# Optimization experiments

Measured on AMD Instinct MI355X. Metric: run time of the kernel, lower is better.

Reference implementation:

```python
import jax, jax.numpy as jnp
import numpy as np

B, T, C, H = 2, 2048, 1024, 16
D = C // H  # 64 per-head dim


def setup_inputs() -> dict:
    key = jax.random.key(0)
    ks = jax.random.split(key, 9)
    s = 1.0 / np.sqrt(C)
    return {
        "query_src": jax.random.normal(ks[0], (B, T, C), jnp.float32),
        "key_src": jax.random.normal(ks[1], (B, T, C), jnp.float32),
        "value_src": jax.random.normal(ks[2], (B, T, C), jnp.float32),
        "Wq": jax.random.normal(ks[3], (C, C), jnp.float32) * s,
        "Wk": jax.random.normal(ks[4], (C, C), jnp.float32) * s,
        "Wv": jax.random.normal(ks[5], (C, C), jnp.float32) * s,
        "Wo": jax.random.normal(ks[6], (C, C), jnp.float32) * s,
        "bo": jax.random.normal(ks[7], (C,), jnp.float32) * s,
    }


def reference(query_src, key_src, value_src, Wq, Wk, Wv, Wo, bo):
    # Linear layers: y = x @ W.T (torch nn.Linear convention)
    q = jnp.einsum('btc,dc->btd', query_src, Wq).reshape(B, T, H, D).transpose(0, 2, 1, 3)
    k = jnp.einsum('btc,dc->btd', key_src, Wk).reshape(B, T, H, D).transpose(0, 2, 1, 3)
    v = jnp.einsum('btc,dc->btd', value_src, Wv).reshape(B, T, H, D).transpose(0, 2, 1, 3)
    # scores: [B, H, T, T]
    scores = jnp.einsum('bhqd,bhkd->bhqk', q, k)
    # FAITHFUL quirk: original divides by d**(-0.5) => multiplies by sqrt(D)
    scores = scores * jnp.sqrt(jnp.asarray(D, scores.dtype))
    # FAITHFUL quirk: softmax over dim=1 == the HEAD axis
    attn = jax.nn.softmax(scores, axis=1)
    # dropout is identity in eval mode
    out = jnp.einsum('bhqk,bhkd->bhqd', attn, v)  # [B,H,T,D]
    out = out.transpose(0, 2, 1, 3).reshape(B, T, C)
    return jnp.einsum('btc,dc->btd', out, Wo) + bo
```

## Files before the change

kernel.cpp:

```cpp
#include <hip/hip_runtime.h>
#include <cmath>

namespace {

constexpr int B_ = 2;
constexpr int T_ = 2048;
constexpr int C_ = 1024;
constexpr int H_ = 16;
constexpr int D_ = 64;

typedef _Float16 half8 __attribute__((ext_vector_type(8)));
typedef _Float16 half4 __attribute__((ext_vector_type(4)));
typedef float f32x4 __attribute__((ext_vector_type(4)));

__device__ inline f32x4 vmax4(f32x4 a, f32x4 b) {
  f32x4 r;
  r[0] = fmaxf(a[0], b[0]); r[1] = fmaxf(a[1], b[1]);
  r[2] = fmaxf(a[2], b[2]); r[3] = fmaxf(a[3], b[3]);
  return r;
}

__device__ __forceinline__ void gload16(const _Float16* g, _Float16* l) {
  __builtin_amdgcn_global_load_lds(
      (const __attribute__((address_space(1))) unsigned int*)g,
      (__attribute__((address_space(3))) unsigned int*)l, 16, 0, 0);
}

__device__ __forceinline__ void lds_barrier() {
  __builtin_amdgcn_sched_barrier(0);
  asm volatile("s_waitcnt lgkmcnt(0)" ::: "memory");
  __builtin_amdgcn_s_barrier();
  __builtin_amdgcn_sched_barrier(0);
}

__global__ __launch_bounds__(256)
void cast7(const float* __restrict__ xq, const float* __restrict__ xk,
           const float* __restrict__ xv, const float* __restrict__ wq,
           const float* __restrict__ wk, const float* __restrict__ wv,
           const float* __restrict__ wo,
           _Float16* __restrict__ dxq, _Float16* __restrict__ dxk,
           _Float16* __restrict__ dxv, _Float16* __restrict__ dwq,
           _Float16* __restrict__ dwk, _Float16* __restrict__ dwv,
           _Float16* __restrict__ dwo) {
  constexpr size_t NX = (size_t)4 << 20;
  constexpr size_t NW = (size_t)1 << 20;
  size_t g = ((size_t)blockIdx.x * 256 + threadIdx.x) * 8;
  const float* s; _Float16* d; size_t off;
  if      (g <     NX)          { s = xq; d = dxq; off = g; }
  else if (g < 2 * NX)          { s = xk; d = dxk; off = g - NX; }
  else if (g < 3 * NX)          { s = xv; d = dxv; off = g - 2 * NX; }
  else if (g < 3 * NX + NW)     { s = wq; d = dwq; off = g - 3 * NX; }
  else if (g < 3 * NX + 2 * NW) { s = wk; d = dwk; off = g - 3 * NX - NW; }
  else if (g < 3 * NX + 3 * NW) { s = wv; d = dwv; off = g - 3 * NX - 2 * NW; }
  else                          { s = wo; d = dwo; off = g - 3 * NX - 3 * NW; }
  const float4 a = *(const float4*)(s + off);
  const float4 b = *(const float4*)(s + off + 4);
  half8 h;
  h[0] = (_Float16)a.x; h[1] = (_Float16)a.y; h[2] = (_Float16)a.z; h[3] = (_Float16)a.w;
  h[4] = (_Float16)b.x; h[5] = (_Float16)b.y; h[6] = (_Float16)b.z; h[7] = (_Float16)b.w;
  *(half8*)(d + off) = h;
}

__global__ __launch_bounds__(256, 3)
void gemm_f16nt(const _Float16* __restrict__ A0, const _Float16* __restrict__ A1,
                const _Float16* __restrict__ A2,
                const _Float16* __restrict__ W0, const _Float16* __restrict__ W1,
                const _Float16* __restrict__ W2,
                _Float16* __restrict__ Y0, _Float16* __restrict__ Y1,
                _Float16* __restrict__ Y2,
                float* __restrict__ Yf, const float* __restrict__ bias,
                int K, int N, int mode, float qsc) {
  __shared__ _Float16 sA[128 * 32];
  __shared__ _Float16 sW[128 * 32];

  const int tid  = threadIdx.x;
  const int lane = tid & 63;
  const int w    = tid >> 6;
  const int l15  = lane & 15;
  const int quad = lane >> 4;
  const int z    = blockIdx.z;
  const _Float16* A = (z == 0) ? A0 : (z == 1) ? A1 : A2;
  const _Float16* W = (z == 0) ? W0 : (z == 1) ? W1 : W2;
  _Float16*       Y = (z == 0) ? Y0 : (z == 1) ? Y1 : Y2;

  const int m0 = blockIdx.y * 128;
  const int n0 = blockIdx.x * 128;

  const int Rb  = lane >> 2;
  const int pch = lane & 3;
  const int lch = pch ^ ((Rb >> 1) & 3);
  const int swr = (l15 >> 1) & 3;

  f32x4 acc[4][4];
#pragma unroll
  for (int mt = 0; mt < 4; ++mt)
#pragma unroll
    for (int nt = 0; nt < 4; ++nt)
      acc[mt][nt] = (f32x4){0.f, 0.f, 0.f, 0.f};

  const int wm = (w >> 1) * 64;
  const int wn = (w & 1) * 64;

  for (int k0 = 0; k0 < K; k0 += 32) {
    __syncthreads();
#pragma unroll
    for (int j = 0; j < 2; ++j) {
      const int seg = w * 32 + j * 16;
      gload16(A + (size_t)(m0 + seg + Rb) * K + k0 + lch * 8, &sA[seg * 32]);
      gload16(W + (size_t)(n0 + seg + Rb) * K + k0 + lch * 8, &sW[seg * 32]);
    }
    __syncthreads();

    half8 af[4], wf[4];
#pragma unroll
    for (int mt = 0; mt < 4; ++mt) {
      const int R = wm + mt * 16 + l15;
      af[mt] = *(const half8*)&sA[R * 32 + (quad ^ swr) * 8];
    }
#pragma unroll
    for (int nt = 0; nt < 4; ++nt) {
      const int R = wn + nt * 16 + l15;
      wf[nt] = *(const half8*)&sW[R * 32 + (quad ^ swr) * 8];
    }
#pragma unroll
    for (int mt = 0; mt < 4; ++mt)
#pragma unroll
      for (int nt = 0; nt < 4; ++nt)
        acc[mt][nt] = __builtin_amdgcn_mfma_f32_16x16x32_f16(wf[nt], af[mt], acc[mt][nt], 0, 0, 0);
  }

  const float ysc = (mode == 0 && z == 0) ? qsc : 1.f;
#pragma unroll
  for (int mt = 0; mt < 4; ++mt)
#pragma unroll
    for (int nt = 0; nt < 4; ++nt) {
      const int m = m0 + wm + mt * 16 + l15;
      const int n = n0 + wn + nt * 16 + quad * 4;
      if (mode == 2) {
        float4 v;
        v.x = acc[mt][nt][0] + bias[n + 0];
        v.y = acc[mt][nt][1] + bias[n + 1];
        v.z = acc[mt][nt][2] + bias[n + 2];
        v.w = acc[mt][nt][3] + bias[n + 3];
        *(float4*)(Yf + (size_t)m * N + n) = v;
      } else {
        half4 hv;
#pragma unroll
        for (int r = 0; r < 4; ++r) hv[r] = (_Float16)(acc[mt][nt][r] * ysc);
        *(half4*)(Y + (size_t)m * N + n) = hv;
      }
    }
}

__global__ __launch_bounds__(256)
void transpose_v(const _Float16* __restrict__ Vh, _Float16* __restrict__ Vt) {
  constexpr int PAD = 1028;
  __shared__ _Float16 tile[16][PAD];
  const int b  = blockIdx.x >> 7;
  const int kt = blockIdx.x & 127;
  const int tid = threadIdx.x;

#pragma unroll
  for (int j = 0; j < 8; ++j) {
    const int ch = tid + 256 * j;
    const int t  = ch >> 7;
    const int c8 = ch & 127;
    *(half8*)&tile[t][c8 * 8] =
        *(const half8*)(Vh + ((size_t)b * T_ + kt * 16 + t) * C_ + c8 * 8);
  }
  __syncthreads();

#pragma unroll
  for (int j = 0; j < 8; ++j) {
    const int cc = tid + 256 * j;
    const int h  = cc >> 7;
    const int d  = (cc >> 1) & 63;
    const int th = (cc & 1) * 8;
    const int c  = h * 64 + d;
    half4 va, vb4;
#pragma unroll
    for (int i = 0; i < 4; ++i) va[i]  = tile[th + i][c];
#pragma unroll
    for (int i = 0; i < 4; ++i) vb4[i] = tile[th + 4 + i][c];
    const size_t base = (((size_t)b * H_ + h) * 128 + kt) * 1024 +
                        (size_t)((d & 15) * 64 + (th >> 2) * 16 + (d >> 4) * 4);
    *(half4*)(Vt + base) = va;
    *(half4*)(Vt + base + 16) = vb4;
  }
}

__global__ __launch_bounds__(256, 2)
void attn_mfma(const _Float16* __restrict__ Qhp, const _Float16* __restrict__ Khp,
               const _Float16* __restrict__ Vtp, _Float16* __restrict__ OP,
               int nsplit) {
  __shared__ f32x4 red[2][2][4][64];

  const int tid  = threadIdx.x;
  const int lane = tid & 63;
  const int w    = tid >> 6;
  const int l15  = lane & 15;
  const int quad = lane >> 4;
  const int cell = quad * 16 + l15;

  const int nbq   = B_ * (T_ / 16);
  const int split = blockIdx.x / nbq;
  const int bq    = blockIdx.x % nbq;
  const int b  = bq >> 7;
  const int q0 = (bq & 127) << 4;

  const size_t qrow = ((size_t)b * T_ + q0 + l15) * C_;

  half8 qh[4][2];
#pragma unroll
  for (int hl = 0; hl < 4; ++hl)
#pragma unroll
    for (int kk = 0; kk < 2; ++kk)
      qh[hl][kk] = *(const half8*)(Qhp + qrow + (w * 4 + hl) * 64 + kk * 32 + quad * 8);

  f32x4 oacc[4][4];
#pragma unroll
  for (int hl = 0; hl < 4; ++hl)
#pragma unroll
    for (int mt = 0; mt < 4; ++mt)
      oacc[hl][mt] = (f32x4){0.f, 0.f, 0.f, 0.f};

  const int kpb  = T_ / nsplit;
  const int k_lo = split * kpb;
  const int jt   = kpb / 16;

  const _Float16* vbase = Vtp + ((size_t)b * H_ + w * 4) * (128 * 1024) +
                          (size_t)(l15 * 64 + quad * 16);

  half8 akA[4][2], akB[4][2];

  auto loadK = [&](half8 (&buf)[4][2], int k0) {
    const size_t krow = ((size_t)b * T_ + k0 + l15) * C_;
#pragma unroll
    for (int hl = 0; hl < 4; ++hl)
#pragma unroll
      for (int kk = 0; kk < 2; ++kk)
        buf[hl][kk] = *(const half8*)(Khp + krow + (w * 4 + hl) * 64 + kk * 32 + quad * 8);
  };

  auto tile = [&](int j, half8 (&cur)[4][2], half8 (&nxt)[4][2]) {
    const int k0 = k_lo + j * 16;
    const int kt = k0 >> 4;
    const int p  = j & 1;

    f32x4 s[4];
#pragma unroll
    for (int hl = 0; hl < 4; ++hl) s[hl] = (f32x4){0.f, 0.f, 0.f, 0.f};
    __builtin_amdgcn_s_setprio(1);
#pragma unroll
    for (int hl = 0; hl < 4; ++hl)
#pragma unroll
      for (int kk = 0; kk < 2; ++kk)
        s[hl] = __builtin_amdgcn_mfma_f32_16x16x32_f16(cur[hl][kk], qh[hl][kk], s[hl], 0, 0, 0);
    __builtin_amdgcn_s_setprio(0);

    half8 avh[4][2];
#pragma unroll
    for (int hl = 0; hl < 4; ++hl) {
      const _Float16* vb = vbase + (size_t)hl * (128 * 1024) + (size_t)kt * 1024;
      avh[hl][0] = *(const half8*)(vb);
      avh[hl][1] = *(const half8*)(vb + 8);
    }
    __builtin_amdgcn_sched_barrier(0);
    if (j + 1 < jt) loadK(nxt, k0 + 16);
    __builtin_amdgcn_sched_barrier(0);

    red[p][0][w][cell] = vmax4(vmax4(s[0], s[1]), vmax4(s[2], s[3]));
    lds_barrier();
    const f32x4 gmax = vmax4(vmax4(red[p][0][0][cell], red[p][0][1][cell]),
                             vmax4(red[p][0][2][cell], red[p][0][3][cell]));
    f32x4 ps = (f32x4){0.f, 0.f, 0.f, 0.f};
#pragma unroll
    for (int hl = 0; hl < 4; ++hl)
#pragma unroll
      for (int r = 0; r < 4; ++r) {
        const float ev = __expf(s[hl][r] - gmax[r]);
        s[hl][r] = ev;
        ps[r] += ev;
      }
    red[p][1][w][cell] = ps;
    lds_barrier();
    const f32x4 gs = red[p][1][0][cell] + red[p][1][1][cell] +
                     red[p][1][2][cell] + red[p][1][3][cell];
    f32x4 inv;
#pragma unroll
    for (int r = 0; r < 4; ++r) inv[r] = 1.f / gs[r];

    half4 pf[4];
#pragma unroll
    for (int hl = 0; hl < 4; ++hl)
#pragma unroll
      for (int r = 0; r < 4; ++r)
        pf[hl][r] = (_Float16)(s[hl][r] * inv[r]);

    __builtin_amdgcn_s_setprio(1);
#pragma unroll
    for (int hl = 0; hl < 4; ++hl) {
      const half4 v0 = __builtin_shufflevector(avh[hl][0], avh[hl][0], 0, 1, 2, 3);
      const half4 v1 = __builtin_shufflevector(avh[hl][0], avh[hl][0], 4, 5, 6, 7);
      const half4 v2 = __builtin_shufflevector(avh[hl][1], avh[hl][1], 0, 1, 2, 3);
      const half4 v3 = __builtin_shufflevector(avh[hl][1], avh[hl][1], 4, 5, 6, 7);
      oacc[hl][0] = __builtin_amdgcn_mfma_f32_16x16x16f16(v0, pf[hl], oacc[hl][0], 0, 0, 0);
      oacc[hl][1] = __builtin_amdgcn_mfma_f32_16x16x16f16(v1, pf[hl], oacc[hl][1], 0, 0, 0);
      oacc[hl][2] = __builtin_amdgcn_mfma_f32_16x16x16f16(v2, pf[hl], oacc[hl][2], 0, 0, 0);
      oacc[hl][3] = __builtin_amdgcn_mfma_f32_16x16x16f16(v3, pf[hl], oacc[hl][3], 0, 0, 0);
    }
    __builtin_amdgcn_s_setprio(0);
  };

  loadK(akA, k_lo);
  for (int j = 0; j < jt; j += 2) {
    tile(j,     akA, akB);
    tile(j + 1, akB, akA);
  }

  _Float16* op = OP + (size_t)split * ((size_t)B_ * T_ * C_);
  const size_t orow = ((size_t)b * T_ + q0 + l15) * C_;
#pragma unroll
  for (int hl = 0; hl < 4; ++hl)
#pragma unroll
    for (int mt = 0; mt < 4; ++mt) {
      half4 hv;
#pragma unroll
      for (int r = 0; r < 4; ++r) hv[r] = (_Float16)oacc[hl][mt][r];
      *(half4*)(op + orow + (w * 4 + hl) * 64 + mt * 16 + quad * 4) = hv;
    }
}

__global__ __launch_bounds__(256)
void reduce_oh(const _Float16* __restrict__ OP, _Float16* __restrict__ AOh,
               int nsplit, size_t n) {
  const size_t i = ((size_t)blockIdx.x * 256 + threadIdx.x) * 8;
  float a[8] = {};
  for (int s = 0; s < nsplit; ++s) {
    const half8 v = *(const half8*)(OP + (size_t)s * n + i);
#pragma unroll
    for (int r = 0; r < 8; ++r) a[r] += (float)v[r];
  }
  half8 o;
#pragma unroll
  for (int r = 0; r < 8; ++r) o[r] = (_Float16)a[r];
  *(half8*)(AOh + i) = o;
}

}

extern "C" void kernel_launch(void* const* d_in, const int* in_sizes, int n_in,
                              void* d_out, int out_size, void* d_ws, size_t ws_size,
                              hipStream_t stream) {
  const float* xq = (const float*)d_in[0];
  const float* xk = (const float*)d_in[1];
  const float* xv = (const float*)d_in[2];
  const float* Wq = (const float*)d_in[3];
  const float* Wk = (const float*)d_in[4];
  const float* Wv = (const float*)d_in[5];
  const float* Wo = (const float*)d_in[6];
  const float* bo = (const float*)d_in[7];
  float* out = (float*)d_out;

  const size_t MB   = 1ull << 20;
  const size_t nBTC = (size_t)B_ * T_ * C_;

  char* wsb = (char*)d_ws;
  _Float16* Qh  = (_Float16*)(wsb + 0 * MB);
  _Float16* Kh  = (_Float16*)(wsb + 8 * MB);
  _Float16* Vt  = (_Float16*)(wsb + 16 * MB);
  _Float16* vh  = (_Float16*)(wsb + 24 * MB);
  _Float16* AOh = (_Float16*)(wsb + 24 * MB);
  _Float16* xqh = (_Float16*)(wsb + 32 * MB);
  _Float16* xkh = (_Float16*)(wsb + 40 * MB);
  _Float16* xvh = (_Float16*)(wsb + 48 * MB);
  _Float16* OP  = (_Float16*)(wsb + 32 * MB);
  _Float16* Wqh = (_Float16*)(wsb + 64 * MB);
  _Float16* Wkh = (_Float16*)(wsb + 66 * MB);
  _Float16* Wvh = (_Float16*)(wsb + 68 * MB);
  _Float16* Woh = (_Float16*)(wsb + 70 * MB);

  const int nsplit = 4;
  const int M = B_ * T_;
  dim3 blk(256);

  cast7<<<dim3(8192), blk, 0, stream>>>(xq, xk, xv, Wq, Wk, Wv, Wo,
                                        xqh, xkh, xvh, Wqh, Wkh, Wvh, Woh);

  gemm_f16nt<<<dim3(C_ / 128, M / 128, 3), blk, 0, stream>>>(
      xqh, xkh, xvh, Wqh, Wkh, Wvh, Qh, Kh, vh,
      nullptr, nullptr, C_, C_, 0, 8.f);

  transpose_v<<<dim3(B_ * 128), blk, 0, stream>>>(vh, Vt);

  attn_mfma<<<dim3(B_ * (T_ / 16) * nsplit), blk, 0, stream>>>(Qh, Kh, Vt, OP, nsplit);

  reduce_oh<<<dim3((unsigned)(nBTC / 2048)), blk, 0, stream>>>(OP, AOh, nsplit, nBTC);

  gemm_f16nt<<<dim3(C_ / 128, M / 128, 1), blk, 0, stream>>>(
      AOh, nullptr, nullptr, Woh, nullptr, nullptr, nullptr, nullptr, nullptr,
      out, bo, C_, C_, 2, 1.f);
}
```

Measured before the change: 424.3 us.

## Remap attention blocks per XCD for L2 reuse and drop K double-buffering

```diff
diff --git a/kernel.cpp b/kernel.cpp
--- a/kernel.cpp
+++ b/kernel.cpp
@@ -24,13 +24,6 @@
   __builtin_amdgcn_global_load_lds(
       (const __attribute__((address_space(1))) unsigned int*)g,
       (__attribute__((address_space(3))) unsigned int*)l, 16, 0, 0);
-}
-
-__device__ __forceinline__ void lds_barrier() {
-  __builtin_amdgcn_sched_barrier(0);
-  asm volatile("s_waitcnt lgkmcnt(0)" ::: "memory");
-  __builtin_amdgcn_s_barrier();
-  __builtin_amdgcn_sched_barrier(0);
 }
 
 __global__ __launch_bounds__(256)
@@ -191,8 +184,7 @@
 
 __global__ __launch_bounds__(256, 2)
 void attn_mfma(const _Float16* __restrict__ Qhp, const _Float16* __restrict__ Khp,
-               const _Float16* __restrict__ Vtp, _Float16* __restrict__ OP,
-               int nsplit) {
+               const _Float16* __restrict__ Vtp, _Float16* __restrict__ OP) {
   __shared__ f32x4 red[2][2][4][64];
 
   const int tid  = threadIdx.x;
@@ -202,11 +194,11 @@
   const int quad = lane >> 4;
   const int cell = quad * 16 + l15;
 
-  const int nbq   = B_ * (T_ / 16);
-  const int split = blockIdx.x / nbq;
-  const int bq    = blockIdx.x % nbq;
-  const int b  = bq >> 7;
-  const int q0 = (bq & 127) << 4;
+  const int xcd   = blockIdx.x & 7;
+  const int qi    = blockIdx.x >> 3;
+  const int b     = xcd & 1;
+  const int split = xcd >> 1;
+  const int q0    = qi << 4;
 
   const size_t qrow = ((size_t)b * T_ + q0 + l15) * C_;
 
@@ -215,7 +207,8 @@
   for (int hl = 0; hl < 4; ++hl)
 #pragma unroll
     for (int kk = 0; kk < 2; ++kk)
-      qh[hl][kk] = *(const half8*)(Qhp + qrow + (w * 4 + hl) * 64 + kk * 32 + quad * 8);
+      qh[hl][kk] = __builtin_nontemporal_load(
+          (const half8*)(Qhp + qrow + (w * 4 + hl) * 64 + kk * 32 + quad * 8));
 
   f32x4 oacc[4][4];
 #pragma unroll
@@ -224,53 +217,46 @@
     for (int mt = 0; mt < 4; ++mt)
       oacc[hl][mt] = (f32x4){0.f, 0.f, 0.f, 0.f};
 
-  const int kpb  = T_ / nsplit;
+  const int kpb  = T_ / 4;
   const int k_lo = split * kpb;
   const int jt   = kpb / 16;
 
   const _Float16* vbase = Vtp + ((size_t)b * H_ + w * 4) * (128 * 1024) +
                           (size_t)(l15 * 64 + quad * 16);
 
-  half8 akA[4][2], akB[4][2];
-
-  auto loadK = [&](half8 (&buf)[4][2], int k0) {
-    const size_t krow = ((size_t)b * T_ + k0 + l15) * C_;
-#pragma unroll
-    for (int hl = 0; hl < 4; ++hl)
-#pragma unroll
-      for (int kk = 0; kk < 2; ++kk)
-        buf[hl][kk] = *(const half8*)(Khp + krow + (w * 4 + hl) * 64 + kk * 32 + quad * 8);
-  };
-
-  auto tile = [&](int j, half8 (&cur)[4][2], half8 (&nxt)[4][2]) {
+  for (int j = 0; j < jt; ++j) {
     const int k0 = k_lo + j * 16;
     const int kt = k0 >> 4;
     const int p  = j & 1;
-
-    f32x4 s[4];
-#pragma unroll
-    for (int hl = 0; hl < 4; ++hl) s[hl] = (f32x4){0.f, 0.f, 0.f, 0.f};
-    __builtin_amdgcn_s_setprio(1);
+    const size_t krow = ((size_t)b * T_ + k0 + l15) * C_;
+
+    half8 akh[4][2];
+    half8 avh[4][2];
 #pragma unroll
     for (int hl = 0; hl < 4; ++hl)
 #pragma unroll
       for (int kk = 0; kk < 2; ++kk)
-        s[hl] = __builtin_amdgcn_mfma_f32_16x16x32_f16(cur[hl][kk], qh[hl][kk], s[hl], 0, 0, 0);
-    __builtin_amdgcn_s_setprio(0);
-
-    half8 avh[4][2];
+        akh[hl][kk] = *(const half8*)(Khp + krow + (w * 4 + hl) * 64 + kk * 32 + quad * 8);
 #pragma unroll
     for (int hl = 0; hl < 4; ++hl) {
       const _Float16* vb = vbase + (size_t)hl * (128 * 1024) + (size_t)kt * 1024;
       avh[hl][0] = *(const half8*)(vb);
       avh[hl][1] = *(const half8*)(vb + 8);
     }
-    __builtin_amdgcn_sched_barrier(0);
-    if (j + 1 < jt) loadK(nxt, k0 + 16);
-    __builtin_amdgcn_sched_barrier(0);
+
+    f32x4 s[4];
+#pragma unroll
+    for (int hl = 0; hl < 4; ++hl) s[hl] = (f32x4){0.f, 0.f, 0.f, 0.f};
+    __builtin_amdgcn_s_setprio(1);
+#pragma unroll
+    for (int hl = 0; hl < 4; ++hl)
+#pragma unroll
+      for (int kk = 0; kk < 2; ++kk)
+        s[hl] = __builtin_amdgcn_mfma_f32_16x16x32_f16(akh[hl][kk], qh[hl][kk], s[hl], 0, 0, 0);
+    __builtin_amdgcn_s_setprio(0);
 
     red[p][0][w][cell] = vmax4(vmax4(s[0], s[1]), vmax4(s[2], s[3]));
-    lds_barrier();
+    __syncthreads();
     const f32x4 gmax = vmax4(vmax4(red[p][0][0][cell], red[p][0][1][cell]),
                              vmax4(red[p][0][2][cell], red[p][0][3][cell]));
     f32x4 ps = (f32x4){0.f, 0.f, 0.f, 0.f};
@@ -283,7 +269,7 @@
         ps[r] += ev;
       }
     red[p][1][w][cell] = ps;
-    lds_barrier();
+    __syncthreads();
     const f32x4 gs = red[p][1][0][cell] + red[p][1][1][cell] +
                      red[p][1][2][cell] + red[p][1][3][cell];
     f32x4 inv;
@@ -310,12 +296,6 @@
       oacc[hl][3] = __builtin_amdgcn_mfma_f32_16x16x16f16(v3, pf[hl], oacc[hl][3], 0, 0, 0);
     }
     __builtin_amdgcn_s_setprio(0);
-  };
-
-  loadK(akA, k_lo);
-  for (int j = 0; j < jt; j += 2) {
-    tile(j,     akA, akB);
-    tile(j + 1, akB, akA);
   }
 
   _Float16* op = OP + (size_t)split * ((size_t)B_ * T_ * C_);
@@ -327,7 +307,8 @@
       half4 hv;
 #pragma unroll
       for (int r = 0; r < 4; ++r) hv[r] = (_Float16)oacc[hl][mt][r];
-      *(half4*)(op + orow + (w * 4 + hl) * 64 + mt * 16 + quad * 4) = hv;
+      __builtin_nontemporal_store(
+          hv, (half4*)(op + orow + (w * 4 + hl) * 64 + mt * 16 + quad * 4));
     }
 }
 
@@ -393,7 +374,7 @@
 
   transpose_v<<<dim3(B_ * 128), blk, 0, stream>>>(vh, Vt);
 
-  attn_mfma<<<dim3(B_ * (T_ / 16) * nsplit), blk, 0, stream>>>(Qh, Kh, Vt, OP, nsplit);
+  attn_mfma<<<dim3(B_ * (T_ / 16) * nsplit), blk, 0, stream>>>(Qh, Kh, Vt, OP);
 
   reduce_oh<<<dim3((unsigned)(nBTC / 2048)), blk, 0, stream>>>(OP, AOh, nsplit, nBTC);
 
```

Measured after the change: 430.4 us. No clear change (+1.4%).
